# Performance work log

Hardware: AMD Instinct MI355X
Metric: run time of the kernel (lower is better)

The kernel has to match this reference:

```python
import jax, jax.numpy as jnp
import numpy as np
from jax import lax

VOCAB = 32000
D = 1024
MASK_ID = 31999
EXPAND_ID = 31998
STEPS = 4
TOP_P = 0.9
TOP_K = 50
NEG = jnp.finfo(jnp.float32).min


def setup_inputs() -> dict:
    key = jax.random.key(0)
    k1, k2, k3, k4 = jax.random.split(key, 4)
    B, S = 2, 512
    # prompt tokens in the first half, mask tokens in the second half
    x = jax.random.randint(k1, (B, S), 0, EXPAND_ID, dtype=jnp.int32)
    x = x.at[:, S // 2:].set(MASK_ID)
    emb = jax.random.normal(k2, (VOCAB, D), jnp.float32) * 0.02
    W1 = jax.random.normal(k3, (D, D), jnp.float32) * 0.02
    Wout = jax.random.normal(k4, (D, VOCAB), jnp.float32) * 0.02
    return {"x": x, "emb": emb, "W1": W1, "Wout": Wout}


def _model_logits(x, emb, W1, Wout):
    # stand-in for DreamOnModel forward: embed -> tanh(dense) -> lm head
    h = emb[x]                        # [B, S, D]
    h = jnp.tanh(h @ W1)              # [B, S, D]
    return h @ Wout                   # [B, S, V]


def _filter_logits(logits):
    # top-p (nucleus) filtering, vectorized over [B, S, V].
    # torch scatters the removal mask back via sorted_indices; with distinct
    # float logits this is equivalent to thresholding at the smallest kept logit.
    sl = jnp.sort(logits, axis=-1)[..., ::-1]                 # descending
    cum = jnp.cumsum(jax.nn.softmax(sl, axis=-1), axis=-1)
    remove = cum > TOP_P
    remove = jnp.concatenate(
        [jnp.zeros_like(remove[..., :1]), remove[..., :-1]], axis=-1)
    keep = jnp.sum(~remove, axis=-1)                          # >= 1 per row
    thr_p = jnp.take_along_axis(sl, (keep - 1)[..., None], axis=-1)
    logits = jnp.where(logits < thr_p, NEG, logits)
    # top-k filtering
    kth = lax.top_k(logits, TOP_K)[0][..., -1:]
    return jnp.where(logits < kth, NEG, logits)


def _diffusion_step(x, emb, W1, Wout):
    mask = x == MASK_ID                                        # [B, S]
    logits = _model_logits(x, emb, W1, Wout)
    # shift-right with duplicated first position (logits predict next token)
    logits = jnp.concatenate([logits[:, :1], logits[:, :-1]], axis=1)
    # penalize expand token (torch applies it on masked rows only; only
    # masked rows are ever consumed, so applying everywhere is equivalent)
    logits = logits.at[..., EXPAND_ID].add(-1e9)
    logits = _filter_logits(logits)
    probs = jax.nn.softmax(logits, axis=-1)
    # temperature == 0 path of sample_tokens: greedy max + confidence
    conf = jnp.max(probs, axis=-1)                             # [B, S]
    x0 = jnp.argmax(probs, axis=-1).astype(x.dtype)            # [B, S]
    # only masked positions compete; transfer exactly 1 token globally
    conf_m = jnp.where(mask, conf, -jnp.inf).reshape(-1)
    idx = jnp.argmax(conf_m)
    any_mask = jnp.any(mask)
    xf = x.reshape(-1)
    x_new = xf.at[idx].set(x0.reshape(-1)[idx])
    x_new = jnp.where(any_mask, x_new, xf).reshape(x.shape)
    return x_new, conf_m[idx]


def reference(x, emb, W1, Wout):
    def body(carry, _):
        x_new, c = _diffusion_step(carry, emb, W1, Wout)
        return x_new, c
    x_final, confs = lax.scan(body, x, None, length=STEPS)
    return x_final, confs
```

## Files before the change

kernel.cpp:

```cpp
#include <hip/hip_runtime.h>
#include <math.h>

#define VOCAB 32000
#define DIM 1024
#define SS 512
#define BS 1024
#define MASK_ID 31999
#define EXPAND_ID 31998
#define NSTEPS 4
#define TOPK 50
#define PW 4
#define ROWS 16
#define KC 16
#define NDCL 16
#define NCH 500
#define THRRANK 49
#define CAP 768
#define NEGF (-3.4028234663852886e38f)

__device__ int   g_x[BS];
__device__ int   g_tok[ROWS];
__device__ int   g_ntok;
__device__ int   g_pbase;
__device__ int   g_pn;
__device__ float g_hp[KC][PW][DIM];
__device__ float g_lpart[NDCL][PW][VOCAB];
__device__ float g_rows[ROWS][VOCAB];
__device__ float g_cmax[ROWS][NCH];
__device__ int   g_camax[ROWS][NCH];
__device__ float g_cz[ROWS][NCH];
__device__ int   g_rowx0[ROWS];
__device__ float g_rowconf[ROWS];

__device__ inline unsigned keyf(float f) {
    unsigned b = __float_as_uint(f);
    return b ^ ((b & 0x80000000u) ? 0xFFFFFFFFu : 0x80000000u);
}

__global__ __launch_bounds__(1024) void k_start(const int* __restrict__ x) {
    int p = threadIdx.x;
    g_x[p] = x[p];
    if (p < ROWS) g_tok[p] = -1;
    __syncthreads();
    if (g_x[p] == MASK_ID) {
        int s = p & (SS - 1);
        int t = g_x[(s == 0) ? p : p - 1];
        for (int r = 0; r < PW; r++) {
            int old = atomicCAS(&g_tok[r], -1, t);
            if (old == -1 || old == t) break;
        }
    }
    __syncthreads();
    if (p == 0) {
        int n = 0;
        while (n < PW && g_tok[n] >= 0) n++;
        g_pbase = 0; g_pn = n; g_ntok = n;
    }
}

__global__ __launch_bounds__(128) void k_h_part(const float* __restrict__ emb,
                                                const float* __restrict__ W1) {
    __shared__ float se[PW][64];
    __shared__ int s_pn, s_pb;
    int tid = threadIdx.x;
    if (tid == 0) { s_pn = g_pn; s_pb = g_pbase; }
    __syncthreads();
    const int pn = s_pn;
    if (pn == 0) return;
    int col = blockIdx.x * 128 + tid;
    int kc = blockIdx.y, dbase = kc * 64;
    for (int i = tid; i < PW * 64; i += 128) {
        int j = i >> 6, dd = i & 63;
        se[j][dd] = (j < pn) ? emb[(size_t)g_tok[s_pb + j] * DIM + dbase + dd] : 0.f;
    }
    __syncthreads();
    float acc[PW] = {0.f, 0.f, 0.f, 0.f};
    #pragma unroll 4
    for (int dd = 0; dd < 64; dd++) {
        float w = W1[(size_t)(dbase + dd) * DIM + col];
        #pragma unroll
        for (int j = 0; j < PW; j++) acc[j] += se[j][dd] * w;
    }
    #pragma unroll
    for (int j = 0; j < PW; j++) g_hp[kc][j][col] = acc[j];
}

template<int NA>
__device__ __forceinline__ void accumL(const float* __restrict__ Wout,
                                       const float (*sh)[64], int dc, int c) {
    float4 acc[NA];
    #pragma unroll
    for (int r = 0; r < NA; r++) acc[r] = make_float4(0.f, 0.f, 0.f, 0.f);
    const float* W = Wout + (size_t)dc * 64 * VOCAB + c;
    #pragma unroll 4
    for (int dd = 0; dd < 64; dd++) {
        float4 w = *(const float4*)(W + (size_t)dd * VOCAB);
        #pragma unroll
        for (int r = 0; r < NA; r++) {
            float s = sh[r][dd];
            acc[r].x += s * w.x; acc[r].y += s * w.y;
            acc[r].z += s * w.z; acc[r].w += s * w.w;
        }
    }
    #pragma unroll
    for (int r = 0; r < NA; r++)
        *(float4*)&g_lpart[dc][r][c] = acc[r];
}

__global__ __launch_bounds__(128) void k_logits(const float* __restrict__ Wout) {
    __shared__ float sh[PW][64];
    __shared__ int s_pn;
    int tid = threadIdx.x, dc = blockIdx.y;
    if (tid == 0) s_pn = g_pn;
    __syncthreads();
    const int pn = s_pn;
    if (pn == 0) return;
    for (int i = tid; i < PW * 64; i += 128) {
        int j = i >> 6, dd = i & 63;
        float s = 0.f;
        if (j < pn) {
            int col = dc * 64 + dd;
            #pragma unroll
            for (int kc = 0; kc < KC; kc++) s += g_hp[kc][j][col];
            s = tanhf(s);
        }
        sh[j][dd] = s;
    }
    __syncthreads();
    int c = blockIdx.x * 512 + tid * 4;
    if (c >= VOCAB) return;
    switch (pn) {
        case 1: accumL<1>(Wout, sh, dc, c); break;
        case 2: accumL<2>(Wout, sh, dc, c); break;
        case 3: accumL<3>(Wout, sh, dc, c); break;
        default: accumL<PW>(Wout, sh, dc, c); break;
    }
}

__global__ __launch_bounds__(256) void k_comb_stats() {
    int j = blockIdx.y;
    if (j >= g_pn) return;
    int slot = g_pbase + j;
    int wv = threadIdx.x >> 6, lane = threadIdx.x & 63;
    int chunk = blockIdx.x * 4 + wv;
    int c = chunk * 64 + lane;
    float v = 0.f;
    #pragma unroll
    for (int dc = 0; dc < NDCL; dc++) v += g_lpart[dc][j][c];
    if (c == EXPAND_ID) v -= 1e9f;
    g_rows[slot][c] = v;
    float bv = v; int bi = c;
    #pragma unroll
    for (int off = 1; off < 64; off <<= 1) {
        float ov = __shfl_xor(bv, off, 64);
        int   oi = __shfl_xor(bi, off, 64);
        if (ov > bv || (ov == bv && oi < bi)) { bv = ov; bi = oi; }
    }
    float z = expf(v - bv);
    #pragma unroll
    for (int off = 1; off < 64; off <<= 1)
        z += __shfl_xor(z, off, 64);
    if (lane == 0) {
        g_cmax[slot][chunk]  = bv;
        g_camax[slot][chunk] = bi;
        g_cz[slot][chunk]    = z;
    }
}

__global__ __launch_bounds__(512) void k_next() {
    __shared__ float rf[512];
    __shared__ int   ri[512];
    __shared__ int s_pn, s_pb;
    int tid = threadIdx.x;
    if (tid == 0) { s_pn = g_pn; s_pb = g_pbase; }
    __syncthreads();
    const int pn = s_pn, base = s_pb;
    for (int j = 0; j < pn; j++) {
        int slot = base + j;
        float bv = NEGF; int bi = 0x7fffffff;
        if (tid < NCH) { bv = g_cmax[slot][tid]; bi = g_camax[slot][tid]; }
        rf[tid] = bv; ri[tid] = bi;
        __syncthreads();
        for (int o = 256; o; o >>= 1) {
            if (tid < o) {
                if (rf[tid + o] > rf[tid] ||
                    (rf[tid + o] == rf[tid] && ri[tid + o] < ri[tid])) {
                    rf[tid] = rf[tid + o]; ri[tid] = ri[tid + o];
                }
            }
            __syncthreads();
        }
        if (tid == 0) g_rowx0[slot] = ri[0];
        __syncthreads();
    }
    if (tid == 0) {
        int nt = g_ntok;
        int nb = nt;
        for (int j = 0; j < pn; j++) {
            int t = g_rowx0[base + j];
            bool found = false;
            for (int k = 0; k < nt; k++) if (g_tok[k] == t) { found = true; break; }
            if (!found && nt < ROWS) g_tok[nt++] = t;
        }
        g_pbase = nb; g_pn = nt - nb; g_ntok = nt;
    }
}

__global__ __launch_bounds__(1024) void k_conf() {
    int slot = blockIdx.x;
    if (slot >= g_pbase) return;
    __shared__ float rf[1024];
    __shared__ float cmv[512];
    __shared__ float cand[CAP];
    __shared__ float sorted_[TOPK];
    __shared__ int s_n;
    __shared__ float s_mx, s_Z;
    __shared__ unsigned s_thr;
    int tid = threadIdx.x;
    rf[tid] = (tid < NCH) ? g_cmax[slot][tid] : NEGF;
    __syncthreads();
    for (int o = 512; o; o >>= 1) {
        if (tid < o) rf[tid] = fmaxf(rf[tid], rf[tid + o]);
        __syncthreads();
    }
    if (tid == 0) s_mx = rf[0];
    __syncthreads();
    float mx = s_mx;
    rf[tid] = (tid < NCH) ? g_cz[slot][tid] * expf(g_cmax[slot][tid] - mx) : 0.f;
    __syncthreads();
    for (int o = 512; o; o >>= 1) {
        if (tid < o) rf[tid] += rf[tid + o];
        __syncthreads();
    }
    if (tid == 0) { s_Z = rf[0]; s_n = 0; }
    __syncthreads();
    if (tid < 512) cmv[tid] = (tid < NCH) ? g_cmax[slot][tid] : NEGF;
    __syncthreads();
    if (tid < NCH) {
        unsigned kt = keyf(cmv[tid]);
        int rank = 0;
        for (int j = 0; j < NCH; j++) {
            unsigned kj = keyf(cmv[j]);
            rank += (kj > kt) || (kj == kt && j < tid);
        }
        if (rank == THRRANK) s_thr = kt;
    }
    __syncthreads();
    unsigned T = s_thr;
    const float4* L4 = (const float4*)g_rows[slot];
    for (int i = tid; i < VOCAB / 4; i += 1024) {
        float4 v4 = L4[i];
        float vv[4] = {v4.x, v4.y, v4.z, v4.w};
        #pragma unroll
        for (int q = 0; q < 4; q++) {
            if (keyf(vv[q]) >= T) {
                int j = atomicAdd(&s_n, 1);
                if (j < CAP) cand[j] = vv[q];
            }
        }
    }
    __syncthreads();
    int n = s_n; if (n > CAP) n = CAP;
    for (int i = tid; i < n; i += 1024) {
        unsigned ki = keyf(cand[i]);
        int rank = 0;
        for (int j = 0; j < n; j++) {
            unsigned kj = keyf(cand[j]);
            rank += (kj > ki) || (kj == ki && j < i);
        }
        if (rank < TOPK) sorted_[rank] = cand[i];
    }
    __syncthreads();
    if (tid == 0) {
        int m = n; if (m > TOPK) m = TOPK;
        float run = expf(sorted_[0] - mx);
        float lim = 0.9f * s_Z;
        for (int j = 1; j < m; j++) {
            if (run > lim) break;
            run += expf(sorted_[j] - mx);
        }
        g_rowconf[slot] = 1.0f / run;
    }
}

__global__ __launch_bounds__(1024) void k_select(float* __restrict__ out) {
    __shared__ int   xl[BS];
    __shared__ float rf[1024];
    __shared__ int   ri[1024];
    __shared__ int   px0[BS];
    __shared__ int   rtok[ROWS];
    __shared__ float rcf[ROWS];
    __shared__ int   rx0[ROWS];
    __shared__ float stepc[NSTEPS];
    __shared__ int s_nt;
    int p = threadIdx.x;
    xl[p] = g_x[p];
    if (p < ROWS) { rtok[p] = g_tok[p]; rcf[p] = g_rowconf[p]; rx0[p] = g_rowx0[p]; }
    if (p == 0) s_nt = g_pbase;
    __syncthreads();
    const int nt = s_nt;
    for (int step = 0; step < NSTEPS; step++) {
        float mc = NEGF; int mx0 = 0;
        if (xl[p] == MASK_ID) {
            int s = p & (SS - 1);
            int t = xl[(s == 0) ? p : p - 1];
            for (int k = 0; k < nt; k++) {
                if (rtok[k] == t) { mc = rcf[k]; mx0 = rx0[k]; break; }
            }
        }
        px0[p] = mx0;
        rf[p] = mc; ri[p] = p;
        __syncthreads();
        for (int o = 512; o; o >>= 1) {
            if (p < o) {
                if (rf[p + o] > rf[p] ||
                    (rf[p + o] == rf[p] && ri[p + o] < ri[p])) {
                    rf[p] = rf[p + o]; ri[p] = ri[p + o];
                }
            }
            __syncthreads();
        }
        if (p == 0) {
            stepc[step] = rf[0];
            if (rf[0] > 0.f) xl[ri[0]] = px0[ri[0]];
        }
        __syncthreads();
    }
    out[p] = (float)xl[p];
    if (p < NSTEPS) out[BS + p] = stepc[p];
}

extern "C" void kernel_launch(void* const* d_in, const int* in_sizes, int n_in,
                              void* d_out, int out_size, void* d_ws, size_t ws_size,
                              hipStream_t stream) {
    const int*   x    = (const int*)  d_in[0];
    const float* emb  = (const float*)d_in[1];
    const float* W1   = (const float*)d_in[2];
    const float* Wout = (const float*)d_in[3];
    float*       out  = (float*)d_out;

    k_start<<<1, 1024, 0, stream>>>(x);
    for (int pass = 0; pass < NSTEPS; pass++) {
        k_h_part<<<dim3(8, KC), 128, 0, stream>>>(emb, W1);
        k_logits<<<dim3(63, NDCL), 128, 0, stream>>>(Wout);
        k_comb_stats<<<dim3(125, PW), 256, 0, stream>>>();
        k_next<<<1, 512, 0, stream>>>();
    }
    k_conf<<<ROWS, 1024, 0, stream>>>();
    k_select<<<1, 1024, 0, stream>>>(out);
}
```

Measured before the change: 229.8 us.

## Fuse next-token and select stages into last-block tails, reduce h in-block

Merges k_next into k_comb_stats and k_select into k_conf using a last-block-done atomic counter, so the tail block does the follow-up work. Computes the hidden layer with a full in-block K reduction plus tanh in k_h, which removes the 16-way partial buffer and its reduction inside k_logits. Together these cut four launches per run and shrink intermediate traffic. In exchange there are threadfence/atomic costs, serial tail work inside the last block, and a 32-block hidden-layer kernel with lower parallelism.

Result: slower. 448.3 us (+95.1%).

```diff
diff --git a/kernel.cpp b/kernel.cpp
--- a/kernel.cpp
+++ b/kernel.cpp
@@ -11,11 +11,11 @@
 #define TOPK 50
 #define PW 4
 #define ROWS 16
-#define KC 16
 #define NDCL 16
 #define NCH 500
 #define THRRANK 49
 #define CAP 768
+#define COMB_BLOCKS 500
 #define NEGF (-3.4028234663852886e38f)
 
 __device__ int   g_x[BS];
@@ -23,7 +23,7 @@
 __device__ int   g_ntok;
 __device__ int   g_pbase;
 __device__ int   g_pn;
-__device__ float g_hp[KC][PW][DIM];
+__device__ float g_h[PW][DIM];
 __device__ float g_lpart[NDCL][PW][VOCAB];
 __device__ float g_rows[ROWS][VOCAB];
 __device__ float g_cmax[ROWS][NCH];
@@ -31,6 +31,8 @@
 __device__ float g_cz[ROWS][NCH];
 __device__ int   g_rowx0[ROWS];
 __device__ float g_rowconf[ROWS];
+__device__ int   g_done;
+__device__ int   g_done2;
 
 __device__ inline unsigned keyf(float f) {
     unsigned b = __float_as_uint(f);
@@ -41,6 +43,7 @@
     int p = threadIdx.x;
     g_x[p] = x[p];
     if (p < ROWS) g_tok[p] = -1;
+    if (p == 0) { g_done = 0; g_done2 = 0; }
     __syncthreads();
     if (g_x[p] == MASK_ID) {
         int s = p & (SS - 1);
@@ -58,31 +61,42 @@
     }
 }
 
-__global__ __launch_bounds__(128) void k_h_part(const float* __restrict__ emb,
-                                                const float* __restrict__ W1) {
-    __shared__ float se[PW][64];
-    __shared__ int s_pn, s_pb;
-    int tid = threadIdx.x;
+__global__ __launch_bounds__(1024) void k_h(const float* __restrict__ emb,
+                                            const float* __restrict__ W1) {
+    __shared__ int   s_pn, s_pb;
+    __shared__ float se[PW][DIM];
+    __shared__ float red[32][33];
+    int tid = threadIdx.x, bid = blockIdx.x;
     if (tid == 0) { s_pn = g_pn; s_pb = g_pbase; }
     __syncthreads();
     const int pn = s_pn;
     if (pn == 0) return;
-    int col = blockIdx.x * 128 + tid;
-    int kc = blockIdx.y, dbase = kc * 64;
-    for (int i = tid; i < PW * 64; i += 128) {
-        int j = i >> 6, dd = i & 63;
-        se[j][dd] = (j < pn) ? emb[(size_t)g_tok[s_pb + j] * DIM + dbase + dd] : 0.f;
-    }
-    __syncthreads();
+    for (int i = tid; i < pn * DIM; i += 1024) {
+        int j = i >> 10, d = i & (DIM - 1);
+        se[j][d] = emb[(size_t)g_tok[s_pb + j] * DIM + d];
+    }
+    __syncthreads();
+    const int ct = tid & 31, kg = tid >> 5;
+    const int col = bid * 32 + ct;
     float acc[PW] = {0.f, 0.f, 0.f, 0.f};
     #pragma unroll 4
-    for (int dd = 0; dd < 64; dd++) {
-        float w = W1[(size_t)(dbase + dd) * DIM + col];
-        #pragma unroll
-        for (int j = 0; j < PW; j++) acc[j] += se[j][dd] * w;
-    }
-    #pragma unroll
-    for (int j = 0; j < PW; j++) g_hp[kc][j][col] = acc[j];
+    for (int dd = 0; dd < 32; dd++) {
+        int d = kg * 32 + dd;
+        float w = W1[(size_t)d * DIM + col];
+        #pragma unroll
+        for (int j = 0; j < PW; j++)
+            if (j < pn) acc[j] += se[j][d] * w;
+    }
+    for (int j = 0; j < pn; j++) {
+        red[kg][ct] = acc[j];
+        __syncthreads();
+        for (int o = 16; o; o >>= 1) {
+            if (kg < o) red[kg][ct] += red[kg + o][ct];
+            __syncthreads();
+        }
+        if (kg == 0) g_h[j][col] = tanhf(red[0][ct]);
+        __syncthreads();
+    }
 }
 
 template<int NA>
@@ -117,14 +131,7 @@
     if (pn == 0) return;
     for (int i = tid; i < PW * 64; i += 128) {
         int j = i >> 6, dd = i & 63;
-        float s = 0.f;
-        if (j < pn) {
-            int col = dc * 64 + dd;
-            #pragma unroll
-            for (int kc = 0; kc < KC; kc++) s += g_hp[kc][j][col];
-            s = tanhf(s);
-        }
-        sh[j][dd] = s;
+        sh[j][dd] = (j < pn) ? g_h[j][dc * 64 + dd] : 0.f;
     }
     __syncthreads();
     int c = blockIdx.x * 512 + tid * 4;
@@ -138,50 +145,54 @@
 }
 
 __global__ __launch_bounds__(256) void k_comb_stats() {
+    __shared__ int s_tail;
+    __shared__ float rf[256];
+    __shared__ int   ri[256];
+    int tid = threadIdx.x;
     int j = blockIdx.y;
-    if (j >= g_pn) return;
-    int slot = g_pbase + j;
-    int wv = threadIdx.x >> 6, lane = threadIdx.x & 63;
-    int chunk = blockIdx.x * 4 + wv;
-    int c = chunk * 64 + lane;
-    float v = 0.f;
-    #pragma unroll
-    for (int dc = 0; dc < NDCL; dc++) v += g_lpart[dc][j][c];
-    if (c == EXPAND_ID) v -= 1e9f;
-    g_rows[slot][c] = v;
-    float bv = v; int bi = c;
-    #pragma unroll
-    for (int off = 1; off < 64; off <<= 1) {
-        float ov = __shfl_xor(bv, off, 64);
-        int   oi = __shfl_xor(bi, off, 64);
-        if (ov > bv || (ov == bv && oi < bi)) { bv = ov; bi = oi; }
-    }
-    float z = expf(v - bv);
-    #pragma unroll
-    for (int off = 1; off < 64; off <<= 1)
-        z += __shfl_xor(z, off, 64);
-    if (lane == 0) {
-        g_cmax[slot][chunk]  = bv;
-        g_camax[slot][chunk] = bi;
-        g_cz[slot][chunk]    = z;
-    }
-}
-
-__global__ __launch_bounds__(512) void k_next() {
-    __shared__ float rf[512];
-    __shared__ int   ri[512];
-    __shared__ int s_pn, s_pb;
-    int tid = threadIdx.x;
-    if (tid == 0) { s_pn = g_pn; s_pb = g_pbase; }
-    __syncthreads();
-    const int pn = s_pn, base = s_pb;
-    for (int j = 0; j < pn; j++) {
+    const int pn = g_pn, base = g_pbase;
+    if (j < pn) {
         int slot = base + j;
+        int wv = tid >> 6, lane = tid & 63;
+        int chunk = blockIdx.x * 4 + wv;
+        int c = chunk * 64 + lane;
+        float v = 0.f;
+        #pragma unroll
+        for (int dc = 0; dc < NDCL; dc++) v += g_lpart[dc][j][c];
+        if (c == EXPAND_ID) v -= 1e9f;
+        g_rows[slot][c] = v;
+        float bv = v; int bi = c;
+        #pragma unroll
+        for (int off = 1; off < 64; off <<= 1) {
+            float ov = __shfl_xor(bv, off, 64);
+            int   oi = __shfl_xor(bi, off, 64);
+            if (ov > bv || (ov == bv && oi < bi)) { bv = ov; bi = oi; }
+        }
+        float z = expf(v - bv);
+        #pragma unroll
+        for (int off = 1; off < 64; off <<= 1)
+            z += __shfl_xor(z, off, 64);
+        if (lane == 0) {
+            g_cmax[slot][chunk]  = bv;
+            g_camax[slot][chunk] = bi;
+            g_cz[slot][chunk]    = z;
+        }
+    }
+    __threadfence();
+    if (tid == 0) s_tail = (atomicAdd(&g_done, 1) == COMB_BLOCKS - 1);
+    __syncthreads();
+    if (!s_tail) return;
+    __threadfence();
+    for (int jj = 0; jj < pn; jj++) {
+        int slot = base + jj;
         float bv = NEGF; int bi = 0x7fffffff;
-        if (tid < NCH) { bv = g_cmax[slot][tid]; bi = g_camax[slot][tid]; }
+        for (int ch = tid; ch < NCH; ch += 256) {
+            float v2 = g_cmax[slot][ch]; int i2 = g_camax[slot][ch];
+            if (v2 > bv || (v2 == bv && i2 < bi)) { bv = v2; bi = i2; }
+        }
         rf[tid] = bv; ri[tid] = bi;
         __syncthreads();
-        for (int o = 256; o; o >>= 1) {
+        for (int o = 128; o; o >>= 1) {
             if (tid < o) {
                 if (rf[tid + o] > rf[tid] ||
                     (rf[tid + o] == rf[tid] && ri[tid + o] < ri[tid])) {
@@ -196,19 +207,18 @@
     if (tid == 0) {
         int nt = g_ntok;
         int nb = nt;
-        for (int j = 0; j < pn; j++) {
-            int t = g_rowx0[base + j];
+        for (int jj = 0; jj < pn; jj++) {
+            int t = g_rowx0[base + jj];
             bool found = false;
             for (int k = 0; k < nt; k++) if (g_tok[k] == t) { found = true; break; }
             if (!found && nt < ROWS) g_tok[nt++] = t;
         }
         g_pbase = nb; g_pn = nt - nb; g_ntok = nt;
-    }
-}
-
-__global__ __launch_bounds__(1024) void k_conf() {
-    int slot = blockIdx.x;
-    if (slot >= g_pbase) return;
+        g_done = 0;
+    }
+}
+
+__global__ __launch_bounds__(1024) void k_conf(float* __restrict__ out) {
     __shared__ float rf[1024];
     __shared__ float cmv[512];
     __shared__ float cand[CAP];
@@ -216,118 +226,124 @@
     __shared__ int s_n;
     __shared__ float s_mx, s_Z;
     __shared__ unsigned s_thr;
+    __shared__ int s_tail;
     int tid = threadIdx.x;
-    rf[tid] = (tid < NCH) ? g_cmax[slot][tid] : NEGF;
-    __syncthreads();
-    for (int o = 512; o; o >>= 1) {
-        if (tid < o) rf[tid] = fmaxf(rf[tid], rf[tid + o]);
-        __syncthreads();
-    }
-    if (tid == 0) s_mx = rf[0];
-    __syncthreads();
-    float mx = s_mx;
-    rf[tid] = (tid < NCH) ? g_cz[slot][tid] * expf(g_cmax[slot][tid] - mx) : 0.f;
-    __syncthreads();
-    for (int o = 512; o; o >>= 1) {
-        if (tid < o) rf[tid] += rf[tid + o];
-        __syncthreads();
-    }
-    if (tid == 0) { s_Z = rf[0]; s_n = 0; }
-    __syncthreads();
-    if (tid < 512) cmv[tid] = (tid < NCH) ? g_cmax[slot][tid] : NEGF;
-    __syncthreads();
-    if (tid < NCH) {
-        unsigned kt = keyf(cmv[tid]);
-        int rank = 0;
-        for (int j = 0; j < NCH; j++) {
-            unsigned kj = keyf(cmv[j]);
-            rank += (kj > kt) || (kj == kt && j < tid);
-        }
-        if (rank == THRRANK) s_thr = kt;
-    }
-    __syncthreads();
-    unsigned T = s_thr;
-    const float4* L4 = (const float4*)g_rows[slot];
-    for (int i = tid; i < VOCAB / 4; i += 1024) {
-        float4 v4 = L4[i];
-        float vv[4] = {v4.x, v4.y, v4.z, v4.w};
-        #pragma unroll
-        for (int q = 0; q < 4; q++) {
-            if (keyf(vv[q]) >= T) {
-                int j = atomicAdd(&s_n, 1);
-                if (j < CAP) cand[j] = vv[q];
-            }
-        }
-    }
-    __syncthreads();
-    int n = s_n; if (n > CAP) n = CAP;
-    for (int i = tid; i < n; i += 1024) {
-        unsigned ki = keyf(cand[i]);
-        int rank = 0;
-        for (int j = 0; j < n; j++) {
-            unsigned kj = keyf(cand[j]);
-            rank += (kj > ki) || (kj == ki && j < i);
-        }
-        if (rank < TOPK) sorted_[rank] = cand[i];
-    }
-    __syncthreads();
-    if (tid == 0) {
-        int m = n; if (m > TOPK) m = TOPK;
-        float run = expf(sorted_[0] - mx);
-        float lim = 0.9f * s_Z;
-        for (int j = 1; j < m; j++) {
-            if (run > lim) break;
-            run += expf(sorted_[j] - mx);
-        }
-        g_rowconf[slot] = 1.0f / run;
-    }
-}
-
-__global__ __launch_bounds__(1024) void k_select(float* __restrict__ out) {
-    __shared__ int   xl[BS];
-    __shared__ float rf[1024];
-    __shared__ int   ri[1024];
-    __shared__ int   px0[BS];
-    __shared__ int   rtok[ROWS];
-    __shared__ float rcf[ROWS];
-    __shared__ int   rx0[ROWS];
-    __shared__ float stepc[NSTEPS];
-    __shared__ int s_nt;
-    int p = threadIdx.x;
-    xl[p] = g_x[p];
-    if (p < ROWS) { rtok[p] = g_tok[p]; rcf[p] = g_rowconf[p]; rx0[p] = g_rowx0[p]; }
-    if (p == 0) s_nt = g_pbase;
-    __syncthreads();
-    const int nt = s_nt;
-    for (int step = 0; step < NSTEPS; step++) {
-        float mc = NEGF; int mx0 = 0;
-        if (xl[p] == MASK_ID) {
-            int s = p & (SS - 1);
-            int t = xl[(s == 0) ? p : p - 1];
-            for (int k = 0; k < nt; k++) {
-                if (rtok[k] == t) { mc = rcf[k]; mx0 = rx0[k]; break; }
-            }
-        }
-        px0[p] = mx0;
-        rf[p] = mc; ri[p] = p;
+    int slot = blockIdx.x;
+    const int nrows = g_pbase;
+    if (slot < nrows) {
+        rf[tid] = (tid < NCH) ? g_cmax[slot][tid] : NEGF;
         __syncthreads();
         for (int o = 512; o; o >>= 1) {
-            if (p < o) {
-                if (rf[p + o] > rf[p] ||
-                    (rf[p + o] == rf[p] && ri[p + o] < ri[p])) {
-                    rf[p] = rf[p + o]; ri[p] = ri[p + o];
+            if (tid < o) rf[tid] = fmaxf(rf[tid], rf[tid + o]);
+            __syncthreads();
+        }
+        if (tid == 0) s_mx = rf[0];
+        __syncthreads();
+        float mx = s_mx;
+        rf[tid] = (tid < NCH) ? g_cz[slot][tid] * expf(g_cmax[slot][tid] - mx) : 0.f;
+        __syncthreads();
+        for (int o = 512; o; o >>= 1) {
+            if (tid < o) rf[tid] += rf[tid + o];
+            __syncthreads();
+        }
+        if (tid == 0) { s_Z = rf[0]; s_n = 0; }
+        __syncthreads();
+        if (tid < 512) cmv[tid] = (tid < NCH) ? g_cmax[slot][tid] : NEGF;
+        __syncthreads();
+        if (tid < NCH) {
+            unsigned kt = keyf(cmv[tid]);
+            int rank = 0;
+            for (int j = 0; j < NCH; j++) {
+                unsigned kj = keyf(cmv[j]);
+                rank += (kj > kt) || (kj == kt && j < tid);
+            }
+            if (rank == THRRANK) s_thr = kt;
+        }
+        __syncthreads();
+        unsigned T = s_thr;
+        const float4* L4 = (const float4*)g_rows[slot];
+        for (int i = tid; i < VOCAB / 4; i += 1024) {
+            float4 v4 = L4[i];
+            float vv[4] = {v4.x, v4.y, v4.z, v4.w};
+            #pragma unroll
+            for (int q = 0; q < 4; q++) {
+                if (keyf(vv[q]) >= T) {
+                    int j = atomicAdd(&s_n, 1);
+                    if (j < CAP) cand[j] = vv[q];
                 }
             }
-            __syncthreads();
-        }
-        if (p == 0) {
-            stepc[step] = rf[0];
-            if (rf[0] > 0.f) xl[ri[0]] = px0[ri[0]];
-        }
-        __syncthreads();
-    }
-    out[p] = (float)xl[p];
-    if (p < NSTEPS) out[BS + p] = stepc[p];
+        }
+        __syncthreads();
+        int n = s_n; if (n > CAP) n = CAP;
+        for (int i = tid; i < n; i += 1024) {
+            unsigned ki = keyf(cand[i]);
+            int rank = 0;
+            for (int j = 0; j < n; j++) {
+                unsigned kj = keyf(cand[j]);
+                rank += (kj > ki) || (kj == ki && j < i);
+            }
+            if (rank < TOPK) sorted_[rank] = cand[i];
+        }
+        __syncthreads();
+        if (tid == 0) {
+            int m = n; if (m > TOPK) m = TOPK;
+            float run = expf(sorted_[0] - s_mx);
+            float lim = 0.9f * s_Z;
+            for (int j = 1; j < m; j++) {
+                if (run > lim) break;
+                run += expf(sorted_[j] - s_mx);
+            }
+            g_rowconf[slot] = 1.0f / run;
+        }
+    }
+    __threadfence();
+    if (tid == 0) s_tail = (atomicAdd(&g_done2, 1) == ROWS - 1);
+    __syncthreads();
+    if (!s_tail) return;
+    __threadfence();
+    {
+        __shared__ int   xl[BS];
+        __shared__ int   ri2[1024];
+        __shared__ int   px0[BS];
+        __shared__ int   rtok[ROWS];
+        __shared__ float rcf[ROWS];
+        __shared__ int   rx0[ROWS];
+        __shared__ float stepc[NSTEPS];
+        int p = tid;
+        xl[p] = g_x[p];
+        if (p < ROWS) { rtok[p] = g_tok[p]; rcf[p] = g_rowconf[p]; rx0[p] = g_rowx0[p]; }
+        __syncthreads();
+        const int nt = nrows;
+        for (int step = 0; step < NSTEPS; step++) {
+            float mc = NEGF; int mx0 = 0;
+            if (xl[p] == MASK_ID) {
+                int s = p & (SS - 1);
+                int t = xl[(s == 0) ? p : p - 1];
+                for (int k = 0; k < nt; k++) {
+                    if (rtok[k] == t) { mc = rcf[k]; mx0 = rx0[k]; break; }
+                }
+            }
+            px0[p] = mx0;
+            rf[p] = mc; ri2[p] = p;
+            __syncthreads();
+            for (int o = 512; o; o >>= 1) {
+                if (p < o) {
+                    if (rf[p + o] > rf[p] ||
+                        (rf[p + o] == rf[p] && ri2[p + o] < ri2[p])) {
+                        rf[p] = rf[p + o]; ri2[p] = ri2[p + o];
+                    }
+                }
+                __syncthreads();
+            }
+            if (p == 0) {
+                stepc[step] = rf[0];
+                if (rf[0] > 0.f) xl[ri2[0]] = px0[ri2[0]];
+            }
+            __syncthreads();
+        }
+        out[p] = (float)xl[p];
+        if (p < NSTEPS) out[BS + p] = stepc[p];
+    }
 }
 
 extern "C" void kernel_launch(void* const* d_in, const int* in_sizes, int n_in,
@@ -341,11 +357,9 @@
 
     k_start<<<1, 1024, 0, stream>>>(x);
     for (int pass = 0; pass < NSTEPS; pass++) {
-        k_h_part<<<dim3(8, KC), 128, 0, stream>>>(emb, W1);
+        k_h<<<32, 1024, 0, stream>>>(emb, W1);
         k_logits<<<dim3(63, NDCL), 128, 0, stream>>>(Wout);
         k_comb_stats<<<dim3(125, PW), 256, 0, stream>>>();
-        k_next<<<1, 512, 0, stream>>>();
-    }
-    k_conf<<<ROWS, 1024, 0, stream>>>();
-    k_select<<<1, 1024, 0, stream>>>(out);
-}
+    }
+    k_conf<<<ROWS, 1024, 0, stream>>>(out);
+}
```

## Reduce hidden layer in-block and fold row argmax into packed atomic key

Applied to the files above, without the earlier changes.

The hidden-layer matmul now does its full K reduction inside each block through a shared-memory tree, and applies tanh there. This removes the partial-sum buffer and the 16-way re-summation and tanh in every logits block. The per-row argmax is now folded into comb_stats as a 64-bit atomicMax on a packed (value key, inverted index) word, so k_next shrinks to a single-thread token-list update. The costs are more synchronizations per hidden block, only 32 blocks for that kernel, and atomic traffic on a few addresses.

Result: slower. 285.4 us (+24.2%).

```diff
diff --git a/kernel.cpp b/kernel.cpp
--- a/kernel.cpp
+++ b/kernel.cpp
@@ -11,7 +11,6 @@
 #define TOPK 50
 #define PW 4
 #define ROWS 16
-#define KC 16
 #define NDCL 16
 #define NCH 500
 #define THRRANK 49
@@ -23,12 +22,12 @@
 __device__ int   g_ntok;
 __device__ int   g_pbase;
 __device__ int   g_pn;
-__device__ float g_hp[KC][PW][DIM];
+__device__ float g_h[PW][DIM];
 __device__ float g_lpart[NDCL][PW][VOCAB];
 __device__ float g_rows[ROWS][VOCAB];
 __device__ float g_cmax[ROWS][NCH];
-__device__ int   g_camax[ROWS][NCH];
 __device__ float g_cz[ROWS][NCH];
+__device__ unsigned long long g_rowkey[ROWS];
 __device__ int   g_rowx0[ROWS];
 __device__ float g_rowconf[ROWS];
 
@@ -40,7 +39,7 @@
 __global__ __launch_bounds__(1024) void k_start(const int* __restrict__ x) {
     int p = threadIdx.x;
     g_x[p] = x[p];
-    if (p < ROWS) g_tok[p] = -1;
+    if (p < ROWS) { g_tok[p] = -1; g_rowkey[p] = 0ull; }
     __syncthreads();
     if (g_x[p] == MASK_ID) {
         int s = p & (SS - 1);
@@ -58,31 +57,42 @@
     }
 }
 
-__global__ __launch_bounds__(128) void k_h_part(const float* __restrict__ emb,
-                                                const float* __restrict__ W1) {
-    __shared__ float se[PW][64];
-    __shared__ int s_pn, s_pb;
-    int tid = threadIdx.x;
+__global__ __launch_bounds__(1024) void k_h(const float* __restrict__ emb,
+                                            const float* __restrict__ W1) {
+    __shared__ int   s_pn, s_pb;
+    __shared__ float se[PW][DIM];
+    __shared__ float red[32][33];
+    int tid = threadIdx.x, bid = blockIdx.x;
     if (tid == 0) { s_pn = g_pn; s_pb = g_pbase; }
     __syncthreads();
     const int pn = s_pn;
     if (pn == 0) return;
-    int col = blockIdx.x * 128 + tid;
-    int kc = blockIdx.y, dbase = kc * 64;
-    for (int i = tid; i < PW * 64; i += 128) {
-        int j = i >> 6, dd = i & 63;
-        se[j][dd] = (j < pn) ? emb[(size_t)g_tok[s_pb + j] * DIM + dbase + dd] : 0.f;
-    }
-    __syncthreads();
+    for (int i = tid; i < pn * DIM; i += 1024) {
+        int j = i >> 10, d = i & (DIM - 1);
+        se[j][d] = emb[(size_t)g_tok[s_pb + j] * DIM + d];
+    }
+    __syncthreads();
+    const int ct = tid & 31, kg = tid >> 5;
+    const int col = bid * 32 + ct;
     float acc[PW] = {0.f, 0.f, 0.f, 0.f};
     #pragma unroll 4
-    for (int dd = 0; dd < 64; dd++) {
-        float w = W1[(size_t)(dbase + dd) * DIM + col];
+    for (int dd = 0; dd < 32; dd++) {
+        int d = kg * 32 + dd;
+        float w = W1[(size_t)d * DIM + col];
         #pragma unroll
-        for (int j = 0; j < PW; j++) acc[j] += se[j][dd] * w;
-    }
-    #pragma unroll
-    for (int j = 0; j < PW; j++) g_hp[kc][j][col] = acc[j];
+        for (int j = 0; j < PW; j++)
+            if (j < pn) acc[j] += se[j][d] * w;
+    }
+    for (int j = 0; j < pn; j++) {
+        red[kg][ct] = acc[j];
+        __syncthreads();
+        for (int o = 16; o; o >>= 1) {
+            if (kg < o) red[kg][ct] += red[kg + o][ct];
+            __syncthreads();
+        }
+        if (kg == 0) g_h[j][col] = tanhf(red[0][ct]);
+        __syncthreads();
+    }
 }
 
 template<int NA>
@@ -117,14 +127,7 @@
     if (pn == 0) return;
     for (int i = tid; i < PW * 64; i += 128) {
         int j = i >> 6, dd = i & 63;
-        float s = 0.f;
-        if (j < pn) {
-            int col = dc * 64 + dd;
-            #pragma unroll
-            for (int kc = 0; kc < KC; kc++) s += g_hp[kc][j][col];
-            s = tanhf(s);
-        }
-        sh[j][dd] = s;
+        sh[j][dd] = (j < pn) ? g_h[j][dc * 64 + dd] : 0.f;
     }
     __syncthreads();
     int c = blockIdx.x * 512 + tid * 4;
@@ -161,49 +164,31 @@
     for (int off = 1; off < 64; off <<= 1)
         z += __shfl_xor(z, off, 64);
     if (lane == 0) {
-        g_cmax[slot][chunk]  = bv;
-        g_camax[slot][chunk] = bi;
-        g_cz[slot][chunk]    = z;
-    }
-}
-
-__global__ __launch_bounds__(512) void k_next() {
-    __shared__ float rf[512];
-    __shared__ int   ri[512];
-    __shared__ int s_pn, s_pb;
-    int tid = threadIdx.x;
-    if (tid == 0) { s_pn = g_pn; s_pb = g_pbase; }
-    __syncthreads();
-    const int pn = s_pn, base = s_pb;
-    for (int j = 0; j < pn; j++) {
-        int slot = base + j;
-        float bv = NEGF; int bi = 0x7fffffff;
-        if (tid < NCH) { bv = g_cmax[slot][tid]; bi = g_camax[slot][tid]; }
-        rf[tid] = bv; ri[tid] = bi;
-        __syncthreads();
-        for (int o = 256; o; o >>= 1) {
-            if (tid < o) {
-                if (rf[tid + o] > rf[tid] ||
-                    (rf[tid + o] == rf[tid] && ri[tid + o] < ri[tid])) {
-                    rf[tid] = rf[tid + o]; ri[tid] = ri[tid + o];
-                }
-            }
-            __syncthreads();
-        }
-        if (tid == 0) g_rowx0[slot] = ri[0];
-        __syncthreads();
-    }
-    if (tid == 0) {
-        int nt = g_ntok;
-        int nb = nt;
-        for (int j = 0; j < pn; j++) {
-            int t = g_rowx0[base + j];
-            bool found = false;
-            for (int k = 0; k < nt; k++) if (g_tok[k] == t) { found = true; break; }
-            if (!found && nt < ROWS) g_tok[nt++] = t;
-        }
-        g_pbase = nb; g_pn = nt - nb; g_ntok = nt;
-    }
+        g_cmax[slot][chunk] = bv;
+        g_cz[slot][chunk]   = z;
+        unsigned long long key =
+            ((unsigned long long)keyf(bv) << 32) |
+            (unsigned long long)(0x7fffffffu - (unsigned)bi);
+        if (key > g_rowkey[slot])
+            atomicMax(&g_rowkey[slot], key);
+    }
+}
+
+__global__ __launch_bounds__(64) void k_next() {
+    if (threadIdx.x != 0) return;
+    int pn = g_pn, base = g_pbase;
+    int nt = g_ntok;
+    int nb = nt;
+    for (int jj = 0; jj < pn; jj++) {
+        int slot = base + jj;
+        unsigned long long key = g_rowkey[slot];
+        int t = (int)(0x7fffffffu - (unsigned)(key & 0xffffffffu));
+        g_rowx0[slot] = t;
+        bool found = false;
+        for (int k = 0; k < nt; k++) if (g_tok[k] == t) { found = true; break; }
+        if (!found && nt < ROWS) g_tok[nt++] = t;
+    }
+    g_pbase = nb; g_pn = nt - nb; g_ntok = nt;
 }
 
 __global__ __launch_bounds__(1024) void k_conf() {
@@ -341,10 +326,10 @@
 
     k_start<<<1, 1024, 0, stream>>>(x);
     for (int pass = 0; pass < NSTEPS; pass++) {
-        k_h_part<<<dim3(8, KC), 128, 0, stream>>>(emb, W1);
+        k_h<<<32, 1024, 0, stream>>>(emb, W1);
         k_logits<<<dim3(63, NDCL), 128, 0, stream>>>(Wout);
         k_comb_stats<<<dim3(125, PW), 256, 0, stream>>>();
-        k_next<<<1, 512, 0, stream>>>();
+        k_next<<<1, 64, 0, stream>>>();
     }
     k_conf<<<ROWS, 1024, 0, stream>>>();
     k_select<<<1, 1024, 0, stream>>>(out);
```

## Fold per-pass argmax into comb_stats atomics and drop k_next kernel

Applied to the files above, without the earlier changes.

Removes the single-block k_next kernel launched every pass by having k_comb_stats publish each chunk's max and index as a packed 64-bit key via atomicMax per row. The next-token set is then rebuilt by a serial closure computed by thread 0 at the start of each k_h_part block and in k_select. This cuts four kernel launches and their serialization, at the cost of redundant serial closure work in every h_part block and global atomics on row keys. Several k_h_part blocks also write g_pn and g_pbase concurrently, all with the same values.

Result: slower. 271.2 us (+18.0%).

```diff
diff --git a/kernel.cpp b/kernel.cpp
--- a/kernel.cpp
+++ b/kernel.cpp
@@ -19,17 +19,16 @@
 #define NEGF (-3.4028234663852886e38f)
 
 __device__ int   g_x[BS];
-__device__ int   g_tok[ROWS];
-__device__ int   g_ntok;
+__device__ int   g_tok[PW];
+__device__ int   g_n1;
+__device__ int   g_pn;
 __device__ int   g_pbase;
-__device__ int   g_pn;
 __device__ float g_hp[KC][PW][DIM];
 __device__ float g_lpart[NDCL][PW][VOCAB];
 __device__ float g_rows[ROWS][VOCAB];
 __device__ float g_cmax[ROWS][NCH];
-__device__ int   g_camax[ROWS][NCH];
 __device__ float g_cz[ROWS][NCH];
-__device__ int   g_rowx0[ROWS];
+__device__ unsigned long long g_rowkey[ROWS];
 __device__ float g_rowconf[ROWS];
 
 __device__ inline unsigned keyf(float f) {
@@ -37,10 +36,30 @@
     return b ^ ((b & 0x80000000u) ? 0xFFFFFFFFu : 0x80000000u);
 }
 
+__device__ inline void closure(int pass, int* toks, int* base_out, int* pn_out) {
+    int n1 = g_n1;
+    for (int i = 0; i < n1; i++) toks[i] = g_tok[i];
+    int base = 0, pn = n1;
+    for (int p = 2; p <= pass; p++) {
+        int nb = base + pn, nn = 0;
+        for (int s = base; s < base + pn; s++) {
+            unsigned long long k = g_rowkey[s];
+            int t = (int)(0x7fffffffu - (unsigned)(k & 0xffffffffu));
+            bool found = false;
+            for (int q = 0; q < nb + nn; q++)
+                if (toks[q] == t) { found = true; break; }
+            if (!found && nb + nn < ROWS) toks[nb + nn++] = t;
+        }
+        base = nb; pn = nn;
+    }
+    *base_out = base; *pn_out = pn;
+}
+
 __global__ __launch_bounds__(1024) void k_start(const int* __restrict__ x) {
     int p = threadIdx.x;
     g_x[p] = x[p];
-    if (p < ROWS) g_tok[p] = -1;
+    if (p < PW) g_tok[p] = -1;
+    if (p < ROWS) g_rowkey[p] = 0ull;
     __syncthreads();
     if (g_x[p] == MASK_ID) {
         int s = p & (SS - 1);
@@ -54,24 +73,31 @@
     if (p == 0) {
         int n = 0;
         while (n < PW && g_tok[n] >= 0) n++;
-        g_pbase = 0; g_pn = n; g_ntok = n;
+        g_n1 = n; g_pn = n; g_pbase = 0;
     }
 }
 
 __global__ __launch_bounds__(128) void k_h_part(const float* __restrict__ emb,
-                                                const float* __restrict__ W1) {
+                                                const float* __restrict__ W1,
+                                                int pass) {
     __shared__ float se[PW][64];
-    __shared__ int s_pn, s_pb;
+    __shared__ int   stoks[ROWS];
+    __shared__ int   s_base, s_pn;
     int tid = threadIdx.x;
-    if (tid == 0) { s_pn = g_pn; s_pb = g_pbase; }
-    __syncthreads();
-    const int pn = s_pn;
+    if (tid == 0) {
+        int b, n;
+        closure(pass, stoks, &b, &n);
+        s_base = b; s_pn = n;
+        g_pn = n; g_pbase = b;
+    }
+    __syncthreads();
+    const int pn = s_pn, base = s_base;
     if (pn == 0) return;
     int col = blockIdx.x * 128 + tid;
     int kc = blockIdx.y, dbase = kc * 64;
     for (int i = tid; i < PW * 64; i += 128) {
         int j = i >> 6, dd = i & 63;
-        se[j][dd] = (j < pn) ? emb[(size_t)g_tok[s_pb + j] * DIM + dbase + dd] : 0.f;
+        se[j][dd] = (j < pn) ? emb[(size_t)stoks[base + j] * DIM + dbase + dd] : 0.f;
     }
     __syncthreads();
     float acc[PW] = {0.f, 0.f, 0.f, 0.f};
@@ -161,54 +187,19 @@
     for (int off = 1; off < 64; off <<= 1)
         z += __shfl_xor(z, off, 64);
     if (lane == 0) {
-        g_cmax[slot][chunk]  = bv;
-        g_camax[slot][chunk] = bi;
-        g_cz[slot][chunk]    = z;
-    }
-}
-
-__global__ __launch_bounds__(512) void k_next() {
-    __shared__ float rf[512];
-    __shared__ int   ri[512];
-    __shared__ int s_pn, s_pb;
-    int tid = threadIdx.x;
-    if (tid == 0) { s_pn = g_pn; s_pb = g_pbase; }
-    __syncthreads();
-    const int pn = s_pn, base = s_pb;
-    for (int j = 0; j < pn; j++) {
-        int slot = base + j;
-        float bv = NEGF; int bi = 0x7fffffff;
-        if (tid < NCH) { bv = g_cmax[slot][tid]; bi = g_camax[slot][tid]; }
-        rf[tid] = bv; ri[tid] = bi;
-        __syncthreads();
-        for (int o = 256; o; o >>= 1) {
-            if (tid < o) {
-                if (rf[tid + o] > rf[tid] ||
-                    (rf[tid + o] == rf[tid] && ri[tid + o] < ri[tid])) {
-                    rf[tid] = rf[tid + o]; ri[tid] = ri[tid + o];
-                }
-            }
-            __syncthreads();
-        }
-        if (tid == 0) g_rowx0[slot] = ri[0];
-        __syncthreads();
-    }
-    if (tid == 0) {
-        int nt = g_ntok;
-        int nb = nt;
-        for (int j = 0; j < pn; j++) {
-            int t = g_rowx0[base + j];
-            bool found = false;
-            for (int k = 0; k < nt; k++) if (g_tok[k] == t) { found = true; break; }
-            if (!found && nt < ROWS) g_tok[nt++] = t;
-        }
-        g_pbase = nb; g_pn = nt - nb; g_ntok = nt;
+        g_cmax[slot][chunk] = bv;
+        g_cz[slot][chunk]   = z;
+        unsigned long long key =
+            ((unsigned long long)keyf(bv) << 32) |
+            (unsigned long long)(0x7fffffffu - (unsigned)bi);
+        if (key > g_rowkey[slot])
+            atomicMax(&g_rowkey[slot], key);
     }
 }
 
 __global__ __launch_bounds__(1024) void k_conf() {
     int slot = blockIdx.x;
-    if (slot >= g_pbase) return;
+    if (slot >= g_pbase + g_pn) return;
     __shared__ float rf[1024];
     __shared__ float cmv[512];
     __shared__ float cand[CAP];
@@ -288,24 +279,32 @@
     __shared__ float rf[1024];
     __shared__ int   ri[1024];
     __shared__ int   px0[BS];
-    __shared__ int   rtok[ROWS];
+    __shared__ int   stoks[ROWS];
     __shared__ float rcf[ROWS];
     __shared__ int   rx0[ROWS];
     __shared__ float stepc[NSTEPS];
     __shared__ int s_nt;
     int p = threadIdx.x;
     xl[p] = g_x[p];
-    if (p < ROWS) { rtok[p] = g_tok[p]; rcf[p] = g_rowconf[p]; rx0[p] = g_rowx0[p]; }
-    if (p == 0) s_nt = g_pbase;
+    if (p == 0) {
+        int b, n;
+        closure(NSTEPS, stoks, &b, &n);
+        s_nt = b + n;
+    }
     __syncthreads();
     const int nt = s_nt;
+    if (p < nt) {
+        rcf[p] = g_rowconf[p];
+        rx0[p] = (int)(0x7fffffffu - (unsigned)(g_rowkey[p] & 0xffffffffu));
+    }
+    __syncthreads();
     for (int step = 0; step < NSTEPS; step++) {
         float mc = NEGF; int mx0 = 0;
         if (xl[p] == MASK_ID) {
             int s = p & (SS - 1);
             int t = xl[(s == 0) ? p : p - 1];
             for (int k = 0; k < nt; k++) {
-                if (rtok[k] == t) { mc = rcf[k]; mx0 = rx0[k]; break; }
+                if (stoks[k] == t) { mc = rcf[k]; mx0 = rx0[k]; break; }
             }
         }
         px0[p] = mx0;
@@ -340,11 +339,10 @@
     float*       out  = (float*)d_out;
 
     k_start<<<1, 1024, 0, stream>>>(x);
-    for (int pass = 0; pass < NSTEPS; pass++) {
-        k_h_part<<<dim3(8, KC), 128, 0, stream>>>(emb, W1);
+    for (int pass = 1; pass <= NSTEPS; pass++) {
+        k_h_part<<<dim3(8, KC), 128, 0, stream>>>(emb, W1, pass);
         k_logits<<<dim3(63, NDCL), 128, 0, stream>>>(Wout);
         k_comb_stats<<<dim3(125, PW), 256, 0, stream>>>();
-        k_next<<<1, 512, 0, stream>>>();
     }
     k_conf<<<ROWS, 1024, 0, stream>>>();
     k_select<<<1, 1024, 0, stream>>>(out);
```
